# Kernel tuning notes

Hardware: AMD Instinct MI355X
Metric: run time of the kernel (lower is better)

The kernel has to match this reference:

```python
import jax, jax.numpy as jnp
import numpy as np

NUM_EMBEDDINGS = 8192
EMBEDDING_DIM = 512
COMMITMENT_COST = 0.25


def setup_inputs() -> dict:
    key = jax.random.key(0)
    kx, ke = jax.random.split(key)
    x = jax.random.normal(kx, (32, 512, EMBEDDING_DIM), dtype=jnp.float32)
    # nn.Embedding weight initialized uniform(-1/K, 1/K)
    emb = jax.random.uniform(ke, (NUM_EMBEDDINGS, EMBEDDING_DIM), dtype=jnp.float32,
                             minval=-1.0 / NUM_EMBEDDINGS, maxval=1.0 / NUM_EMBEDDINGS)
    return {"x": x, "emb": emb}


def reference(x, emb):
    sg = jax.lax.stop_gradient
    D = emb.shape[1]
    flat = x.reshape(-1, D)  # [N, D]
    # squared euclidean distances via ||a||^2 + ||b||^2 - 2 a.b  -> [N, K]
    distances = (jnp.sum(flat ** 2, axis=1, keepdims=True)
                 + jnp.sum(emb ** 2, axis=1)
                 - 2.0 * flat @ emb.T)
    encoding_indices = jnp.argmin(distances, axis=1)  # [N]
    quantized = emb[encoding_indices].reshape(x.shape)
    e_latent_loss = jnp.mean((sg(quantized) - x) ** 2)
    q_latent_loss = jnp.mean((quantized - sg(x)) ** 2)
    loss = q_latent_loss + COMMITMENT_COST * e_latent_loss
    quantized_st = x + sg(quantized - x)  # straight-through estimator
    # Faithful to the original (buggy) perplexity: torch.bincount has length
    # max(idx)+1 = L; mean(counts/N) over L bins == 1/L (a scalar).
    L = (jnp.max(encoding_indices) + 1).astype(x.dtype)
    avg_probs = 1.0 / L
    perplexity = jnp.exp(-avg_probs * jnp.log(avg_probs + 1e-10))
    return quantized_st, loss, perplexity, encoding_indices.reshape(-1, 1)
```

## Files before the change

kernel.cpp:

```cpp
#include <hip/hip_runtime.h>
#include <math.h>

#define N_ROWS   16384
#define DIM      512
#define DQV      128
#define K_CODES  8192
#define NSPLIT   2
#define KHALF    (K_CODES / NSPLIT)
#define BM       64
#define RPW      8
#define BK       512
#define BD       8
#define DCS      (DIM / BD)
#define NSTRIP   (KHALF / BK)
#define THREADS  512
#define EPI_BM   64

#define OUT_LOSS 8388608
#define OUT_PERP 8388609
#define OUT_IDX  8388610

#define WS_XX    0
#define WS_BV0   65536
#define WS_BI0   131072
#define WS_BV1   196608
#define WS_BI1   262144
#define WS_LOSS  327680
#define WS_MAXI  327688

__global__ void init_ws(double* ws_loss, int* ws_maxidx) {
    *ws_loss = 0.0;
    *ws_maxidx = 0;
}

__device__ __forceinline__ float p128_sq(const float4* p) {
    float4 q0 = p[0], q1 = p[1];
    float r0 = __fmul_rn(q0.x, q0.x), r1 = __fmul_rn(q0.y, q0.y);
    float r2 = __fmul_rn(q0.z, q0.z), r3 = __fmul_rn(q0.w, q0.w);
    float r4 = __fmul_rn(q1.x, q1.x), r5 = __fmul_rn(q1.y, q1.y);
    float r6 = __fmul_rn(q1.z, q1.z), r7 = __fmul_rn(q1.w, q1.w);
    #pragma unroll
    for (int t = 1; t < 16; ++t) {
        q0 = p[2 * t]; q1 = p[2 * t + 1];
        r0 = __fadd_rn(r0, __fmul_rn(q0.x, q0.x));
        r1 = __fadd_rn(r1, __fmul_rn(q0.y, q0.y));
        r2 = __fadd_rn(r2, __fmul_rn(q0.z, q0.z));
        r3 = __fadd_rn(r3, __fmul_rn(q0.w, q0.w));
        r4 = __fadd_rn(r4, __fmul_rn(q1.x, q1.x));
        r5 = __fadd_rn(r5, __fmul_rn(q1.y, q1.y));
        r6 = __fadd_rn(r6, __fmul_rn(q1.z, q1.z));
        r7 = __fadd_rn(r7, __fmul_rn(q1.w, q1.w));
    }
    return __fadd_rn(__fadd_rn(__fadd_rn(r0, r1), __fadd_rn(r2, r3)),
                     __fadd_rn(__fadd_rn(r4, r5), __fadd_rn(r6, r7)));
}

__global__ __launch_bounds__(256) void xx_kernel(const float4* __restrict__ x4,
                                                 float* __restrict__ xx) {
    int row = blockIdx.x * 256 + threadIdx.x;
    const float4* p = x4 + (size_t)row * DQV;
    float a = p128_sq(p);
    float b = p128_sq(p + 32);
    float c = p128_sq(p + 64);
    float d = p128_sq(p + 96);
    xx[row] = __fadd_rn(__fadd_rn(a, b), __fadd_rn(c, d));
}

__global__ __launch_bounds__(256) void xt_kernel(const float* __restrict__ x,
                                                 float* __restrict__ xt) {
    __shared__ float t[64][65];
    const int bn = blockIdx.x;
    const int bd = blockIdx.y;
    const int tx = threadIdx.x & 15;
    const int ty = threadIdx.x >> 4;
    #pragma unroll
    for (int i = 0; i < 4; ++i) {
        int nl = 16 * i + ty;
        float4 v = *(const float4*)(x + (size_t)(bn * 64 + nl) * DIM + bd * 64 + 4 * tx);
        t[4 * tx + 0][nl] = v.x;
        t[4 * tx + 1][nl] = v.y;
        t[4 * tx + 2][nl] = v.z;
        t[4 * tx + 3][nl] = v.w;
    }
    __syncthreads();
    #pragma unroll
    for (int i = 0; i < 4; ++i) {
        int dl = 16 * i + ty;
        float4 w;
        w.x = t[dl][4 * tx + 0];
        w.y = t[dl][4 * tx + 1];
        w.z = t[dl][4 * tx + 2];
        w.w = t[dl][4 * tx + 3];
        *(float4*)(xt + (size_t)(bd * 64 + dl) * N_ROWS + bn * 64 + 4 * tx) = w;
    }
}

__global__ __launch_bounds__(THREADS, 2)
void vq_main(const float* __restrict__ xt,
             const float* __restrict__ emb,
             const float* __restrict__ xx,
             float* __restrict__ bv0,
             int* __restrict__ bi0,
             float* __restrict__ bv1,
             int* __restrict__ bi1) {
    __shared__ float Xs[DIM * BM];
    __shared__ float Et[2][BD * BK];

    const int tid  = threadIdx.x;
    const int lane = tid & 63;
    const int wv   = tid >> 6;
    const int wvu  = __builtin_amdgcn_readfirstlane(wv);
    const int rt   = blockIdx.x >> 1;
    const int h    = blockIdx.x & 1;
    const int r0   = rt * BM;
    const int kb   = h * KHALF;
    const int rl   = wvu << 3;
    const int rwu  = r0 + rl;

    const float4* emb4 = (const float4*)emb;
    const float4* xt4  = (const float4*)xt;
    const int cc = tid;

    {
        float4* xs4 = (float4*)Xs;
        #pragma unroll
        for (int it = 0; it < 16; ++it) {
            int i  = it * THREADS + tid;
            int d  = i >> 4;
            int rq = i & 15;
            xs4[i] = xt4[(size_t)d * (N_ROWS / 4) + (r0 >> 2) + rq];
        }
    }

    float bestv[RPW];
    int   besti[RPW];
    #pragma unroll
    for (int i = 0; i < RPW; ++i) { bestv[i] = 3.402823466e38f; besti[i] = 0; }

    float4 pe0, pe1;
    {
        const float4* ep = emb4 + (size_t)(kb + cc) * DQV;
        pe0 = ep[0]; pe1 = ep[1];
    }

    for (int kc = 0; kc < NSTRIP; ++kc) {
        const int k0 = kb + kc * BK;

        float acc[RPW][8];
        #pragma unroll
        for (int i = 0; i < RPW; ++i)
            #pragma unroll
            for (int j = 0; j < 8; ++j) acc[i][j] = 0.0f;

        __syncthreads();
        {
            Et[0][0 * BK + cc] = pe0.x; Et[0][1 * BK + cc] = pe0.y;
            Et[0][2 * BK + cc] = pe0.z; Et[0][3 * BK + cc] = pe0.w;
            Et[0][4 * BK + cc] = pe1.x; Et[0][5 * BK + cc] = pe1.y;
            Et[0][6 * BK + cc] = pe1.z; Et[0][7 * BK + cc] = pe1.w;
        }

        for (int dc = 0; dc < DCS; ++dc) {
            const int buf = dc & 1;
            __syncthreads();

            {
                int nk0, ndq;
                if (dc < DCS - 1) { nk0 = k0; ndq = 2 * (dc + 1); }
                else { nk0 = (kc < NSTRIP - 1) ? k0 + BK : kb; ndq = 0; }
                const float4* ep = emb4 + (size_t)(nk0 + cc) * DQV + ndq;
                pe0 = ep[0]; pe1 = ep[1];
            }

            const int dbase = dc * BD;
            #pragma unroll
            for (int dd = 0; dd < BD; ++dd) {
                float4 xa = *(const float4*)(&Xs[(dbase + dd) * BM + rl]);
                float4 xb = *(const float4*)(&Xs[(dbase + dd) * BM + rl + 4]);
                const float* ep = &Et[buf][dd * BK + 4 * lane];
                float4 e0 = *(const float4*)(ep);
                float4 e1 = *(const float4*)(ep + 256);
                float xs[RPW] = {xa.x, xa.y, xa.z, xa.w, xb.x, xb.y, xb.z, xb.w};
                float ev[8] = {e0.x, e0.y, e0.z, e0.w, e1.x, e1.y, e1.z, e1.w};
                #pragma unroll
                for (int i = 0; i < RPW; ++i)
                    #pragma unroll
                    for (int j = 0; j < 8; ++j)
                        acc[i][j] = __fmaf_rn(xs[i], ev[j], acc[i][j]);
            }

            if (dc < DCS - 1) {
                const int nb = buf ^ 1;
                Et[nb][0 * BK + cc] = pe0.x; Et[nb][1 * BK + cc] = pe0.y;
                Et[nb][2 * BK + cc] = pe0.z; Et[nb][3 * BK + cc] = pe0.w;
                Et[nb][4 * BK + cc] = pe1.x; Et[nb][5 * BK + cc] = pe1.y;
                Et[nb][6 * BK + cc] = pe1.z; Et[nb][7 * BK + cc] = pe1.w;
            }
        }

        #pragma unroll
        for (int i = 0; i < RPW; ++i) {
            float xr_n = xx[rwu + i];
            #pragma unroll
            for (int j2 = 0; j2 < 2; ++j2) {
                #pragma unroll
                for (int t = 0; t < 4; ++t) {
                    float s = __fmaf_rn(-2.0f, acc[i][4 * j2 + t], xr_n);
                    int code = k0 + 256 * j2 + 4 * lane + t;
                    if (s < bestv[i]) { bestv[i] = s; besti[i] = code; }
                }
            }
        }
    }

    #pragma unroll
    for (int i = 0; i < RPW; ++i) {
        float v  = bestv[i];
        int  idx = besti[i];
        #pragma unroll
        for (int off = 32; off > 0; off >>= 1) {
            float vv = __shfl_down(v, off);
            int   ii = __shfl_down(idx, off);
            if (vv < v || (vv == v && ii < idx)) { v = vv; idx = ii; }
        }
        if (lane == 0) {
            if (h == 0) { bv0[rwu + i] = v; bi0[rwu + i] = idx; }
            else        { bv1[rwu + i] = v; bi1[rwu + i] = idx; }
        }
    }
}

__global__ __launch_bounds__(256) void vq_epi(const float* __restrict__ x,
                                              const float* __restrict__ emb,
                                              const float* __restrict__ bv0,
                                              const int* __restrict__ bi0,
                                              const float* __restrict__ bv1,
                                              const int* __restrict__ bi1,
                                              float* __restrict__ out,
                                              double* __restrict__ ws_loss,
                                              int* __restrict__ ws_maxidx) {
    __shared__ int idxRow[EPI_BM];
    const int tid = threadIdx.x;
    const int r0  = blockIdx.x * EPI_BM;
    const float4* x4   = (const float4*)x;
    const float4* emb4 = (const float4*)emb;
    float4*       out4 = (float4*)out;

    if (tid < EPI_BM) {
        int row = r0 + tid;
        float v0 = bv0[row]; int i0 = bi0[row];
        float v1 = bv1[row]; int i1 = bi1[row];
        int idx = (v1 < v0) ? i1 : i0;
        idxRow[tid] = idx;
        out[OUT_IDX + row] = (float)idx;
        atomicMax(ws_maxidx, idx);
    }
    __syncthreads();

    double lsum = 0.0;
    for (int i = tid; i < EPI_BM * DQV; i += 256) {
        int row = i >> 7, dq = i & 127;
        int ki  = idxRow[row];
        float4 q  = emb4[(size_t)ki * DQV + dq];
        float4 xv = x4[(size_t)(r0 + row) * DQV + dq];
        float d0 = q.x - xv.x, d1 = q.y - xv.y, d2 = q.z - xv.z, d3 = q.w - xv.w;
        lsum += (double)d0 * (double)d0 + (double)d1 * (double)d1
              + (double)d2 * (double)d2 + (double)d3 * (double)d3;
        float4 o;
        o.x = xv.x + d0; o.y = xv.y + d1; o.z = xv.z + d2; o.w = xv.w + d3;
        out4[(size_t)(r0 + row) * DQV + dq] = o;
    }
    #pragma unroll
    for (int off = 32; off > 0; off >>= 1) lsum += __shfl_down(lsum, off);
    if ((tid & 63) == 0) atomicAdd(ws_loss, lsum);
}

__global__ void vq_final(const double* __restrict__ ws_loss,
                         const int* __restrict__ ws_maxidx,
                         float* __restrict__ out) {
    if (threadIdx.x == 0) {
        double mean = *ws_loss / (double)((size_t)N_ROWS * DIM);
        out[OUT_LOSS] = (float)(1.25 * mean);
        double L   = (double)(*ws_maxidx + 1);
        double avg = 1.0 / L;
        out[OUT_PERP] = (float)exp(-avg * log(avg + 1e-10));
    }
}

extern "C" void kernel_launch(void* const* d_in, const int* in_sizes, int n_in,
                              void* d_out, int out_size, void* d_ws, size_t ws_size,
                              hipStream_t stream) {
    const float* x   = (const float*)d_in[0];
    const float* emb = (const float*)d_in[1];
    float* out = (float*)d_out;

    char* ws = (char*)d_ws;
    float*  xx        = (float*)(ws + WS_XX);
    float*  bv0       = (float*)(ws + WS_BV0);
    int*    bi0       = (int*)  (ws + WS_BI0);
    float*  bv1       = (float*)(ws + WS_BV1);
    int*    bi1       = (int*)  (ws + WS_BI1);
    double* ws_loss   = (double*)(ws + WS_LOSS);
    int*    ws_maxidx = (int*)  (ws + WS_MAXI);

    float* xt = out;

    hipLaunchKernelGGL(init_ws, dim3(1), dim3(1), 0, stream, ws_loss, ws_maxidx);
    hipLaunchKernelGGL(xx_kernel, dim3(N_ROWS / 256), dim3(256), 0, stream,
                       (const float4*)x, xx);
    hipLaunchKernelGGL(xt_kernel, dim3(N_ROWS / 64, DIM / 64), dim3(256), 0, stream,
                       x, xt);
    hipLaunchKernelGGL(vq_main, dim3((N_ROWS / BM) * NSPLIT), dim3(THREADS), 0, stream,
                       xt, emb, xx, bv0, bi0, bv1, bi1);
    hipLaunchKernelGGL(vq_epi, dim3(N_ROWS / EPI_BM), dim3(256), 0, stream,
                       x, emb, bv0, bi0, bv1, bi1, out, ws_loss, ws_maxidx);
    hipLaunchKernelGGL(vq_final, dim3(1), dim3(64), 0, stream,
                       ws_loss, ws_maxidx, out);
}
```

Baseline: 1.791 ms.

## Stream x tile through double-buffered LDS chunks and raise occupancy target

Replaces the full 64x512 x-tile held in LDS (128 KB) with a small double-buffered 8x64 slice that is prefetched from global memory alongside each embedding chunk. This cuts LDS use per block sharply, so launch bounds are raised to ask for 4 blocks per CU. The cost is reloading x slices from global/L2 on every k-strip (8 times per block instead of once), and the tighter register budget may cause spills given the 64-element accumulator array.

```diff
diff --git a/kernel.cpp b/kernel.cpp
--- a/kernel.cpp
+++ b/kernel.cpp
@@ -95,7 +95,7 @@
     }
 }
 
-__global__ __launch_bounds__(THREADS, 2)
+__global__ __launch_bounds__(THREADS, 4)
 void vq_main(const float* __restrict__ xt,
              const float* __restrict__ emb,
              const float* __restrict__ xx,
@@ -103,8 +103,8 @@
              int* __restrict__ bi0,
              float* __restrict__ bv1,
              int* __restrict__ bi1) {
-    __shared__ float Xs[DIM * BM];
     __shared__ float Et[2][BD * BK];
+    __shared__ float Xs[2][BD * BM];
 
     const int tid  = threadIdx.x;
     const int lane = tid & 63;
@@ -118,19 +118,9 @@
     const int rwu  = r0 + rl;
 
     const float4* emb4 = (const float4*)emb;
-    const float4* xt4  = (const float4*)xt;
     const int cc = tid;
-
-    {
-        float4* xs4 = (float4*)Xs;
-        #pragma unroll
-        for (int it = 0; it < 16; ++it) {
-            int i  = it * THREADS + tid;
-            int d  = i >> 4;
-            int rq = i & 15;
-            xs4[i] = xt4[(size_t)d * (N_ROWS / 4) + (r0 >> 2) + rq];
-        }
-    }
+    const int xd = tid >> 6;
+    const int xr = tid & 63;
 
     float bestv[RPW];
     int   besti[RPW];
@@ -138,9 +128,11 @@
     for (int i = 0; i < RPW; ++i) { bestv[i] = 3.402823466e38f; besti[i] = 0; }
 
     float4 pe0, pe1;
+    float  px;
     {
         const float4* ep = emb4 + (size_t)(kb + cc) * DQV;
         pe0 = ep[0]; pe1 = ep[1];
+        px  = xt[(size_t)xd * N_ROWS + r0 + xr];
     }
 
     for (int kc = 0; kc < NSTRIP; ++kc) {
@@ -158,6 +150,7 @@
             Et[0][2 * BK + cc] = pe0.z; Et[0][3 * BK + cc] = pe0.w;
             Et[0][4 * BK + cc] = pe1.x; Et[0][5 * BK + cc] = pe1.y;
             Et[0][6 * BK + cc] = pe1.z; Et[0][7 * BK + cc] = pe1.w;
+            Xs[0][xd * BM + xr] = px;
         }
 
         for (int dc = 0; dc < DCS; ++dc) {
@@ -165,18 +158,19 @@
             __syncthreads();
 
             {
-                int nk0, ndq;
-                if (dc < DCS - 1) { nk0 = k0; ndq = 2 * (dc + 1); }
-                else { nk0 = (kc < NSTRIP - 1) ? k0 + BK : kb; ndq = 0; }
-                const float4* ep = emb4 + (size_t)(nk0 + cc) * DQV + ndq;
+                int nk0, ndb;
+                if (dc < DCS - 1) { nk0 = k0; ndb = (dc + 1) * BD; }
+                else { nk0 = (kc < NSTRIP - 1) ? k0 + BK : kb; ndb = 0; }
+                const float4* ep = emb4 + (size_t)(nk0 + cc) * DQV + (ndb >> 2);
                 pe0 = ep[0]; pe1 = ep[1];
+                px  = xt[(size_t)(ndb + xd) * N_ROWS + r0 + xr];
             }
 
-            const int dbase = dc * BD;
+            const int dbase_lds = 0;
             #pragma unroll
             for (int dd = 0; dd < BD; ++dd) {
-                float4 xa = *(const float4*)(&Xs[(dbase + dd) * BM + rl]);
-                float4 xb = *(const float4*)(&Xs[(dbase + dd) * BM + rl + 4]);
+                float4 xa = *(const float4*)(&Xs[buf][dd * BM + rl]);
+                float4 xb = *(const float4*)(&Xs[buf][dd * BM + rl + 4]);
                 const float* ep = &Et[buf][dd * BK + 4 * lane];
                 float4 e0 = *(const float4*)(ep);
                 float4 e1 = *(const float4*)(ep + 256);
@@ -188,6 +182,7 @@
                     for (int j = 0; j < 8; ++j)
                         acc[i][j] = __fmaf_rn(xs[i], ev[j], acc[i][j]);
             }
+            (void)dbase_lds;
 
             if (dc < DCS - 1) {
                 const int nb = buf ^ 1;
@@ -195,6 +190,7 @@
                 Et[nb][2 * BK + cc] = pe0.z; Et[nb][3 * BK + cc] = pe0.w;
                 Et[nb][4 * BK + cc] = pe1.x; Et[nb][5 * BK + cc] = pe1.y;
                 Et[nb][6 * BK + cc] = pe1.z; Et[nb][7 * BK + cc] = pe1.w;
+                Xs[nb][xd * BM + xr] = px;
             }
         }
 
```

Result: slower. 2.539 ms (+41.8%).
